# Kernel optimization log

Measured on AMD Instinct MI355X. Metric: run time of the kernel, lower is better.

The kernel has to match this reference:

```python
import jax, jax.numpy as jnp
import numpy as np
jax.config.update("jax_enable_x64", True)

B, S, E, H, L = 2, 1024, 768, 8, 8
FF, V = 2048, 32000
NT, REAL = 1, 512  # n_thoughts_taken, real_token_count


def _ln(x, g, b, eps=1e-5):
    m = jnp.mean(x, axis=-1, keepdims=True)
    v = jnp.var(x, axis=-1, keepdims=True)
    return (x - m) / jnp.sqrt(v + eps) * g + b


def setup_inputs() -> dict:
    key = jax.random.key(0)
    ks = jax.random.split(key, 12)
    f32 = jnp.float32
    rn = lambda k, shp, s=0.02: jax.random.normal(k, shp, f32) * s
    return {
        "x": jax.random.normal(ks[0], (B, S, E), f32),
        "tpe": rn(ks[1], (NT + 1, E)),
        "Wqkv": rn(ks[2], (L, 3 * E, E)),
        "bqkv": jnp.zeros((L, 3 * E), f32),
        "W1": rn(ks[3], (L, FF, E)),
        "b1": jnp.zeros((L, FF), f32),
        "W2": rn(ks[4], (L, E, FF)),
        "b2": jnp.zeros((L, E), f32),
        "g1": jnp.ones((L, E), f32),
        "be1": jnp.zeros((L, E), f32),
        "g2": jnp.ones((L, E), f32),
        "be2": jnp.zeros((L, E), f32),
        "gf": jnp.ones((E,), f32),
        "bf": jnp.zeros((E,), f32),
        "Wp1": rn(ks[5], (FF, E)),
        "bp1": jnp.zeros((FF,), f32),
        "Wp2": rn(ks[6], (V, FF)),
        "bp2": jnp.zeros((V,), f32),
        "Wv1": rn(ks[7], (FF, E)),
        "bv1": jnp.zeros((FF,), f32),
        "Wv2": rn(ks[8], (1, FF)),
        "bv2": jnp.zeros((1,), f32),
        "n_thoughts_taken": NT,
        "real_token_count": REAL,
    }


def reference(x, tpe, Wqkv, bqkv, W1, b1, W2, b2, g1, be1, g2, be2, gf, bf,
              Wp1, bp1, Wp2, bp2, Wv1, bv1, Wv2, bv2,
              n_thoughts_taken, real_token_count):
    Bs, Sq, Em = x.shape
    bs = int(n_thoughts_taken) + 1          # per-thought block size
    real = int(real_token_count)
    dh = Em // H

    # ---- DualPositionalEncoding (dropout=0) ----
    pos = np.arange(real)[:, None]
    div = np.exp(np.arange(0, Em, 2) * (-np.log(10000.0) / Em))
    pe = np.zeros((real, Em), np.float32)
    pe[:, 0::2] = np.sin(pos * div)
    pe[:, 1::2] = np.cos(pos * div)
    xb = x[:, :real * bs].reshape(Bs, real, bs, Em)
    xb = xb + jnp.asarray(pe)[None, :, None, :] + tpe[None, None, :bs, :]
    h = xb.reshape(Bs, real * bs, Em)
    pad = Sq - real * bs
    if pad > 0:
        h = jnp.pad(h, ((0, 0), (0, pad), (0, 0)))

    # ---- block-causal mask. NOTE: the original adds the BOOL mask to the
    # fp64 scores, so masked positions get +1.0 (not -inf). Faithful. ----
    i = np.arange(Sq)
    tok = i // bs
    p = i % bs
    M = ((tok[:, None] == tok[None, :]) & (p[None, :] >= p[:, None])) | \
        ((p[:, None] == 0) & (i[None, :] > i[:, None]) & (i[None, :] < real * bs))
    bias = jnp.asarray((M.T == 0).astype(np.float64))  # [S, S]
    scale = 1.0 / np.sqrt(dh)

    def layer(hc, params):
        Wq, bq, w1, b1_, w2, b2_, g1_, be1_, g2_, be2_ = params
        h64 = hc.astype(jnp.float64)
        qkv = h64 @ Wq.astype(jnp.float64).T + bq.astype(jnp.float64)
        q, k, v = jnp.split(qkv, 3, axis=-1)
        heads = lambda t: t.reshape(Bs, Sq, H, dh).transpose(0, 2, 1, 3)
        q, k, v = heads(q), heads(k), heads(v)
        scores = jnp.einsum('bhqd,bhkd->bhqk', q, k) * scale + bias
        w = jax.nn.softmax(scores, axis=-1)
        o = jnp.einsum('bhqk,bhkd->bhqd', w, v)
        o = o.transpose(0, 2, 1, 3).reshape(Bs, Sq, Em).astype(hc.dtype)
        # NOTE: original skips the attention out_proj entirely. Faithful.
        hc = _ln(hc + o, g1_, be1_)
        ff = jax.nn.gelu(hc @ w1.T + b1_, approximate=False) @ w2.T + b2_
        hc = _ln(hc + ff, g2_, be2_)
        return jnp.nan_to_num(hc), None

    h, _ = jax.lax.scan(layer, h, (Wqkv, bqkv, W1, b1, W2, b2, g1, be1, g2, be2))
    h = _ln(h, gf, bf)  # TransformerEncoder final norm

    act_idx = jnp.arange(real) * bs + n_thoughts_taken
    a = h[:, act_idx]  # [B, real, E]
    policy = jax.nn.gelu(a @ Wp1.T + bp1, approximate=False) @ Wp2.T + bp2
    value = jax.nn.gelu(a @ Wv1.T + bv1, approximate=False) @ Wv2.T + bv2
    return policy, value
```

## Files before the change

### kernel.cpp

```cpp
#include <hip/hip_runtime.h>
#include <math.h>

#define BB    2
#define SS    1024
#define EE    768
#define NH    8
#define DHD   96
#define NL    8
#define FFD   2048
#define VD    32000
#define REALC 512
#define MTOK  (BB*SS)
#define MACTN (BB*REALC)
#define QKVW  (3*EE)

#define QB 64
#define KB 64
#define KS_LD 104
#define VT_LD 72
#define P_LD  72

typedef __attribute__((ext_vector_type(8))) short bf16x8;
typedef __attribute__((ext_vector_type(4))) float f32x4;

static __device__ __forceinline__ float gelu_exact(float x) {
    return 0.5f * x * (1.0f + erff(x * 0.7071067811865476f));
}
static __device__ __forceinline__ unsigned short f2bf(float f) {
    unsigned int u = __builtin_bit_cast(unsigned int, f);
    unsigned int r = u + 0x7FFFu + ((u >> 16) & 1u);
    return (unsigned short)(r >> 16);
}
static __device__ __forceinline__ float bf2f(unsigned short u) {
    union { unsigned int i; float f; } v; v.i = ((unsigned int)u) << 16; return v.f;
}

#define GLDS16(gp, lp) __builtin_amdgcn_global_load_lds( \
    (const __attribute__((address_space(1))) void*)(gp), \
    (__attribute__((address_space(3))) void*)(lp), 16, 0, 0)

#define CN0 (NL*QKVW*EE)
#define CN1 (NL*FFD*EE)
#define CN2 (NL*EE*FFD)
#define CN3 (FFD*EE)
#define CN4 (FFD*EE)
#define CN5 (VD*FFD)
#define CB0 (CN0/4)
#define CB1 (CB0 + CN1/4)
#define CB2 (CB1 + CN2/4)
#define CB3 (CB2 + CN3/4)
#define CB4 (CB3 + CN4/4)
#define CB5 (CB4 + CN5/4)

__global__ __launch_bounds__(256) void convall_kernel(
    const float* __restrict__ s0, const float* __restrict__ s1,
    const float* __restrict__ s2, const float* __restrict__ s3,
    const float* __restrict__ s4, const float* __restrict__ s5,
    unsigned short* __restrict__ dst) {
    int i = blockIdx.x * 256 + threadIdx.x;
    const float* src;
    int loc;
    if      (i < CB0) { src = s0; loc = i; }
    else if (i < CB1) { src = s1; loc = i - CB0; }
    else if (i < CB2) { src = s2; loc = i - CB1; }
    else if (i < CB3) { src = s3; loc = i - CB2; }
    else if (i < CB4) { src = s4; loc = i - CB3; }
    else              { src = s5; loc = i - CB4; }
    float4 v = ((const float4*)src)[loc];
    ushort4 o;
    o.x = f2bf(v.x); o.y = f2bf(v.y); o.z = f2bf(v.z); o.w = f2bf(v.w);
    ((ushort4*)dst)[i] = o;
}

__global__ __launch_bounds__(256) void embed_kernel(const float* __restrict__ x,
                                                    const float* __restrict__ tpe,
                                                    float* __restrict__ h,
                                                    unsigned short* __restrict__ hb) {
    int idx = blockIdx.x * 256 + threadIdx.x;
    if (idx >= MTOK * EE) return;
    int e = idx % EE;
    int tok = idx / EE;
    int s = tok & (SS - 1);
    int r = s >> 1;
    int p = s & 1;
    int k2 = (e >> 1) * 2;
    double div = exp((double)k2 * (-9.210340371976184 / (double)EE));
    double ang = (double)r * div;
    float pe = (e & 1) ? (float)cos(ang) : (float)sin(ang);
    float v = x[idx] + pe + tpe[p * EE + e];
    h[idx] = v;
    hb[idx] = f2bf(v);
}

template<int MODE>
__global__ __launch_bounds__(256) void gemm64_kernel(
    const unsigned short* __restrict__ A, const unsigned short* __restrict__ W,
    const float* __restrict__ bias, float* __restrict__ Cf,
    unsigned short* __restrict__ Cb, unsigned short* __restrict__ CvT,
    int M, int N, int K, int ldc) {
    __shared__ unsigned short As[2][64 * 32];
    __shared__ unsigned short Bs[2][128 * 32];
    const int bm = blockIdx.y * 64;
    const int bn = blockIdx.x * 128;
    const int t = threadIdx.x;
    const int w = t >> 6;
    const int lane = t & 63;
    const int wm = (w >> 1) * 32;
    const int wn = (w & 1) * 64;
    f32x4 acc[2][4] = {};

    const int sr   = t >> 2;
    const int skey = (t >> 3) & 3;
    const int scol = ((t & 3) ^ skey) * 8;
    const unsigned short* gA = A + (size_t)(bm + sr) * K + scol;
    const unsigned short* gB = W + (size_t)(bn + sr) * K + scol;

    const int lc  = lane & 15;
    const int lr4 = lane >> 4;
    const int sl  = (lr4 ^ ((lc >> 1) & 3)) * 8;

    const int nsteps = K >> 5;
    GLDS16(gA,                  &As[0][w * 512]);
    GLDS16(gB,                  &Bs[0][w * 512]);
    GLDS16(gB + (size_t)64 * K, &Bs[0][2048 + w * 512]);
    __syncthreads();
    for (int kt = 0; kt < nsteps; ++kt) {
        const int cur = kt & 1;
        if (kt + 1 < nsteps) {
            const int k0 = (kt + 1) << 5;
            GLDS16(gA + k0,                  &As[cur ^ 1][w * 512]);
            GLDS16(gB + k0,                  &Bs[cur ^ 1][w * 512]);
            GLDS16(gB + (size_t)64 * K + k0, &Bs[cur ^ 1][2048 + w * 512]);
        }
        bf16x8 a[2], b[4];
#pragma unroll
        for (int mi = 0; mi < 2; ++mi)
            a[mi] = *(const bf16x8*)&As[cur][(wm + mi * 16 + lc) * 32 + sl];
#pragma unroll
        for (int ni = 0; ni < 4; ++ni)
            b[ni] = *(const bf16x8*)&Bs[cur][(wn + ni * 16 + lc) * 32 + sl];
#pragma unroll
        for (int mi = 0; mi < 2; ++mi)
#pragma unroll
            for (int ni = 0; ni < 4; ++ni)
                acc[mi][ni] = __builtin_amdgcn_mfma_f32_16x16x32_bf16(
                    a[mi], b[ni], acc[mi][ni], 0, 0, 0);
        __syncthreads();
    }

    const bool vpart = (MODE == 1) && (bn >= 2 * EE);
#pragma unroll
    for (int mi = 0; mi < 2; ++mi) {
#pragma unroll
        for (int ni = 0; ni < 4; ++ni) {
            const int c = bn + wn + ni * 16 + lc;
            const float bv = bias[c];
            const int rwb = bm + wm + mi * 16 + lr4 * 4;
            if (vpart) {
                ushort4 pk;
                pk.x = f2bf(acc[mi][ni][0] + bv);
                pk.y = f2bf(acc[mi][ni][1] + bv);
                pk.z = f2bf(acc[mi][ni][2] + bv);
                pk.w = f2bf(acc[mi][ni][3] + bv);
                *(ushort4*)&CvT[(size_t)(c - 2 * EE) * MTOK + rwb] = pk;
            } else {
#pragma unroll
                for (int r = 0; r < 4; ++r) {
                    float v = acc[mi][ni][r] + bv;
                    if (MODE == 3) {
                        v = gelu_exact(v);
                        Cb[(size_t)(rwb + r) * ldc + c] = f2bf(v);
                    } else if (MODE == 1) {
                        Cb[(size_t)(rwb + r) * ldc + c] = f2bf(v);
                    } else {
                        Cf[(size_t)(rwb + r) * ldc + c] = v;
                    }
                }
            }
        }
    }
}

__global__ __launch_bounds__(256, 2) void gemm_policy_kernel(
    const unsigned short* __restrict__ A, const unsigned short* __restrict__ W,
    const float* __restrict__ bias, float* __restrict__ C, int lda) {
    const int id = blockIdx.x;
    const int xcd = id & 7;
    const int rest = id >> 3;
    const int mt = rest & 7;
    const int ntile = (rest >> 3) * 8 + xcd;
    if (ntile >= VD / 256) return;
    const int bm = mt * 128;
    const int bn = ntile * 256;
    const int K = FFD;

    __shared__ unsigned short As[128 * 64];
    __shared__ unsigned short Bs[256 * 64];
    const int t = threadIdx.x;
    const int w = t >> 6;
    const int lane = t & 63;
    const int wm = (w >> 1) * 64;
    const int wn = (w & 1) * 128;
    f32x4 acc[4][8] = {};

    const int rr8  = (w << 3) + (lane >> 3);
    const int scol = (((lane & 7) ^ ((lane >> 3) & 7))) * 8;
    const unsigned short* gA = A + (size_t)(bm + rr8) * lda + scol;
    const unsigned short* gB = W + (size_t)(bn + rr8) * K + scol;

    const int lc  = lane & 15;
    const int lr4 = lane >> 4;
    const int key8 = lc & 7;

    for (int k0 = 0; k0 < K; k0 += 64) {
        __syncthreads();
#pragma unroll
        for (int i = 0; i < 4; ++i)
            GLDS16(gA + (size_t)(i * 32) * lda + k0, &As[((w << 3) + i * 32) * 64]);
#pragma unroll
        for (int i = 0; i < 8; ++i)
            GLDS16(gB + (size_t)(i * 32) * K + k0, &Bs[((w << 3) + i * 32) * 64]);
        __syncthreads();
#pragma unroll
        for (int ks = 0; ks < 2; ++ks) {
            const int sl = ((ks * 4 + lr4) ^ key8) * 8;
            bf16x8 a[4], b[8];
#pragma unroll
            for (int mi = 0; mi < 4; ++mi)
                a[mi] = *(const bf16x8*)&As[(wm + mi * 16 + lc) * 64 + sl];
#pragma unroll
            for (int ni = 0; ni < 8; ++ni)
                b[ni] = *(const bf16x8*)&Bs[(wn + ni * 16 + lc) * 64 + sl];
#pragma unroll
            for (int mi = 0; mi < 4; ++mi)
#pragma unroll
                for (int ni = 0; ni < 8; ++ni)
                    acc[mi][ni] = __builtin_amdgcn_mfma_f32_16x16x32_bf16(
                        a[mi], b[ni], acc[mi][ni], 0, 0, 0);
        }
    }
#pragma unroll
    for (int mi = 0; mi < 4; ++mi) {
#pragma unroll
        for (int ni = 0; ni < 8; ++ni) {
            const int c = bn + wn + ni * 16 + lc;
            const float bv = bias[c];
            const int rwb = bm + wm + mi * 16 + lr4 * 4;
#pragma unroll
            for (int r = 0; r < 4; ++r)
                C[(size_t)(rwb + r) * VD + c] = acc[mi][ni][r] + bv;
        }
    }
}

__global__ __launch_bounds__(256) void attn_mfma_kernel(
    const unsigned short* __restrict__ qkvb,
    const unsigned short* __restrict__ vT,
    float* __restrict__ o) {
    __shared__ unsigned short Ks[KB * KS_LD];
    __shared__ unsigned short VTs[DHD * VT_LD];
    __shared__ unsigned short Ps[QB * P_LD];

    const int bq = blockIdx.x * QB;
    const int hh = blockIdx.y & 7;
    const int b  = blockIdx.y >> 3;
    const int t = threadIdx.x;
    const int w = t >> 6;
    const int lane = t & 63;
    const int lr = lane >> 4;
    const int lc = lane & 15;
    const float scale = 0.10206207261596577f;

    bf16x8 qa[3];
    {
        const unsigned short* qrow = qkvb + (size_t)(b * SS + bq + w * 16 + lc) * QKVW + hh * DHD;
#pragma unroll
        for (int ks = 0; ks < 3; ++ks)
            qa[ks] = *(const bf16x8*)(qrow + ks * 32 + lr * 8);
    }

    f32x4 acc_o[6] = {};
    float m_st[4], l_st[4];
#pragma unroll
    for (int r = 0; r < 4; ++r) { m_st[r] = -1e30f; l_st[r] = 0.f; }
    const int q_row = lr << 2;

    for (int kt = 0; kt < SS / KB; ++kt) {
        __syncthreads();
#pragma unroll
        for (int it = 0; it < 3; ++it) {
            int flat = it * 256 + t;
            int kr = flat / 12;
            int d8 = (flat % 12) * 8;
            *(bf16x8*)&Ks[kr * KS_LD + d8] =
                *(const bf16x8*)&qkvb[(size_t)(b * SS + kt * KB + kr) * QKVW + EE + hh * DHD + d8];
            int d  = flat >> 3;
            int k8 = (flat & 7) * 8;
            *(bf16x8*)&VTs[d * VT_LD + k8] =
                *(const bf16x8*)&vT[(size_t)(hh * DHD + d) * MTOK + b * SS + kt * KB + k8];
        }
        __syncthreads();

        f32x4 sfr[4] = {};
#pragma unroll
        for (int nf = 0; nf < 4; ++nf) {
#pragma unroll
            for (int ks = 0; ks < 3; ++ks) {
                bf16x8 kb = *(const bf16x8*)&Ks[(nf * 16 + lc) * KS_LD + ks * 32 + lr * 8];
                sfr[nf] = __builtin_amdgcn_mfma_f32_16x16x32_bf16(qa[ks], kb, sfr[nf], 0, 0, 0);
            }
        }
        const int kbase = kt * KB;
#pragma unroll
        for (int nf = 0; nf < 4; ++nf) {
            const int k = kbase + nf * 16 + lc;
#pragma unroll
            for (int r = 0; r < 4; ++r) {
                const int q = bq + w * 16 + q_row + r;
                bool allowed = (((k >> 1) == (q >> 1)) && ((q & 1) >= (k & 1))) ||
                               (((k & 1) == 0) && (q > k));
                sfr[nf][r] = sfr[nf][r] * scale + (allowed ? 0.f : 1.f);
            }
        }
        float corr[4];
#pragma unroll
        for (int r = 0; r < 4; ++r) {
            float v = fmaxf(fmaxf(sfr[0][r], sfr[1][r]), fmaxf(sfr[2][r], sfr[3][r]));
            v = fmaxf(v, __shfl_xor(v, 1)); v = fmaxf(v, __shfl_xor(v, 2));
            v = fmaxf(v, __shfl_xor(v, 4)); v = fmaxf(v, __shfl_xor(v, 8));
            float mn = fmaxf(m_st[r], v);
            corr[r] = __expf(m_st[r] - mn);
            m_st[r] = mn;
        }
        float rsum[4] = {0.f, 0.f, 0.f, 0.f};
#pragma unroll
        for (int nf = 0; nf < 4; ++nf) {
#pragma unroll
            for (int r = 0; r < 4; ++r) {
                float p = __expf(sfr[nf][r] - m_st[r]);
                rsum[r] += p;
                Ps[(w * 16 + q_row + r) * P_LD + nf * 16 + lc] = f2bf(p);
            }
        }
#pragma unroll
        for (int r = 0; r < 4; ++r) {
            float v = rsum[r];
            v += __shfl_xor(v, 1); v += __shfl_xor(v, 2);
            v += __shfl_xor(v, 4); v += __shfl_xor(v, 8);
            l_st[r] = l_st[r] * corr[r] + v;
        }
#pragma unroll
        for (int nf = 0; nf < 6; ++nf)
#pragma unroll
            for (int r = 0; r < 4; ++r)
                acc_o[nf][r] *= corr[r];
#pragma unroll
        for (int ks2 = 0; ks2 < 2; ++ks2) {
            bf16x8 pa = *(const bf16x8*)&Ps[(w * 16 + lc) * P_LD + ks2 * 32 + lr * 8];
#pragma unroll
            for (int nf = 0; nf < 6; ++nf) {
                bf16x8 vb = *(const bf16x8*)&VTs[(nf * 16 + lc) * VT_LD + ks2 * 32 + lr * 8];
                acc_o[nf] = __builtin_amdgcn_mfma_f32_16x16x32_bf16(pa, vb, acc_o[nf], 0, 0, 0);
            }
        }
    }
#pragma unroll
    for (int nf = 0; nf < 6; ++nf) {
#pragma unroll
        for (int r = 0; r < 4; ++r) {
            const int q = bq + w * 16 + q_row + r;
            o[(size_t)(b * SS + q) * EE + hh * DHD + nf * 16 + lc] = acc_o[nf][r] / l_st[r];
        }
    }
}

template<bool GATHER>
__global__ __launch_bounds__(256) void ln_kernel(const float* __restrict__ a,
                                                 const float* __restrict__ res,
                                                 const float* __restrict__ g,
                                                 const float* __restrict__ beta,
                                                 float* __restrict__ outf,
                                                 unsigned short* __restrict__ outb) {
    __shared__ float rs[256], rs2[256];
    const int row = blockIdx.x;
    const int t = threadIdx.x;
    int src = row;
    if (GATHER) src = (row >> 9) * SS + ((row & 511) << 1) + 1;
    const float* pa = a + (size_t)src * EE;
    const float* pr = res ? res + (size_t)src * EE : nullptr;
    float x[3];
    float s = 0.f, s2 = 0.f;
#pragma unroll
    for (int i = 0; i < 3; ++i) {
        int e = t + i * 256;
        float v = pa[e] + (pr ? pr[e] : 0.f);
        x[i] = v; s += v; s2 += v * v;
    }
    rs[t] = s; rs2[t] = s2; __syncthreads();
    for (int k = 128; k > 0; k >>= 1) {
        if (t < k) { rs[t] += rs[t + k]; rs2[t] += rs2[t + k]; }
        __syncthreads();
    }
    const float mean = rs[0] * (1.0f / EE);
    const float var  = rs2[0] * (1.0f / EE) - mean * mean;
    const float rstd = 1.0f / sqrtf(var + 1e-5f);
#pragma unroll
    for (int i = 0; i < 3; ++i) {
        int e = t + i * 256;
        float v = (x[i] - mean) * rstd * g[e] + beta[e];
        if (isnan(v)) v = 0.f;
        if (outf) outf[(size_t)row * EE + e] = v;
        if (outb) outb[(size_t)row * EE + e] = f2bf(v);
    }
}

__global__ __launch_bounds__(256) void value2_kernel(const unsigned short* __restrict__ v1,
                                                     const float* __restrict__ Wv2,
                                                     const float* __restrict__ bv2,
                                                     float* __restrict__ out, int ld) {
    __shared__ float red[256];
    const int row = blockIdx.x;
    const int t = threadIdx.x;
    const unsigned short* pr = v1 + (size_t)row * ld;
    float s = 0.f;
    for (int i = t; i < FFD; i += 256) s = fmaf(bf2f(pr[i]), Wv2[i], s);
    red[t] = s; __syncthreads();
    for (int k = 128; k > 0; k >>= 1) {
        if (t < k) red[t] += red[t + k];
        __syncthreads();
    }
    if (t == 0) out[row] = red[0] + bv2[0];
}

extern "C" void kernel_launch(void* const* d_in, const int* in_sizes, int n_in,
                              void* d_out, int out_size, void* d_ws, size_t ws_size,
                              hipStream_t stream) {
    const float* x    = (const float*)d_in[0];
    const float* tpe  = (const float*)d_in[1];
    const float* Wqkv = (const float*)d_in[2];
    const float* bqkv = (const float*)d_in[3];
    const float* W1   = (const float*)d_in[4];
    const float* b1   = (const float*)d_in[5];
    const float* W2   = (const float*)d_in[6];
    const float* b2   = (const float*)d_in[7];
    const float* g1   = (const float*)d_in[8];
    const float* be1  = (const float*)d_in[9];
    const float* g2   = (const float*)d_in[10];
    const float* be2  = (const float*)d_in[11];
    const float* gf   = (const float*)d_in[12];
    const float* bf   = (const float*)d_in[13];
    const float* Wp1  = (const float*)d_in[14];
    const float* bp1  = (const float*)d_in[15];
    const float* Wp2  = (const float*)d_in[16];
    const float* bp2  = (const float*)d_in[17];
    const float* Wv1  = (const float*)d_in[18];
    const float* bv1  = (const float*)d_in[19];
    const float* Wv2  = (const float*)d_in[20];
    const float* bv2  = (const float*)d_in[21];

    float* ws  = (float*)d_ws;
    float* h   = ws;
    float* o   = h  + (size_t)MTOK * EE;
    float* hc  = o  + (size_t)MTOK * EE;
    float* ff2 = hc + (size_t)MTOK * EE;
    float* bias_cat = ff2 + (size_t)MTOK * EE;
    unsigned short* bws = (unsigned short*)(bias_cat + 4096);
    unsigned short* h_bf    = bws;
    unsigned short* hc_bf   = h_bf    + (size_t)MTOK * EE;
    unsigned short* ff1_bf  = hc_bf   + (size_t)MTOK * EE;
    unsigned short* act_bf  = ff1_bf  + (size_t)MTOK * FFD;
    unsigned short* p1v1_bf = act_bf  + (size_t)MACTN * EE;
    unsigned short* qkv_bf  = p1v1_bf + (size_t)MACTN * 2 * FFD;
    unsigned short* vT      = qkv_bf  + (size_t)MTOK * QKVW;
    unsigned short* wq_all  = vT      + (size_t)EE * MTOK;
    unsigned short* w1_all  = wq_all  + (size_t)CN0;
    unsigned short* w2_all  = w1_all  + (size_t)CN1;
    unsigned short* wp1_bf  = w2_all  + (size_t)CN2;
    unsigned short* wv1_bf  = wp1_bf  + (size_t)CN3;
    unsigned short* wp2_bf  = wv1_bf  + (size_t)CN4;
    (void)wv1_bf;

    float* pol = (float*)d_out;
    float* val = (float*)d_out + (size_t)MACTN * VD;

    const int C256 = 256;
#define NBLK(n) (((n) + 255) / 256)

    embed_kernel<<<NBLK(MTOK * EE), C256, 0, stream>>>(x, tpe, h, h_bf);

    convall_kernel<<<CB5 / 256, C256, 0, stream>>>(Wqkv, W1, W2, Wp1, Wv1, Wp2, wq_all);

    hipMemcpyAsync(bias_cat,        bp1, FFD * sizeof(float), hipMemcpyDeviceToDevice, stream);
    hipMemcpyAsync(bias_cat + FFD,  bv1, FFD * sizeof(float), hipMemcpyDeviceToDevice, stream);

    for (int l = 0; l < NL; ++l) {
        gemm64_kernel<1><<<dim3(QKVW / 128, MTOK / 64), C256, 0, stream>>>(
            h_bf, wq_all + (size_t)l * QKVW * EE, bqkv + (size_t)l * QKVW,
            nullptr, qkv_bf, vT, MTOK, QKVW, EE, QKVW);
        attn_mfma_kernel<<<dim3(SS / QB, BB * NH), C256, 0, stream>>>(qkv_bf, vT, o);
        ln_kernel<false><<<MTOK, C256, 0, stream>>>(h, o, g1 + l * EE, be1 + l * EE, hc, hc_bf);
        gemm64_kernel<3><<<dim3(FFD / 128, MTOK / 64), C256, 0, stream>>>(
            hc_bf, w1_all + (size_t)l * FFD * EE, b1 + (size_t)l * FFD,
            nullptr, ff1_bf, nullptr, MTOK, FFD, EE, FFD);
        gemm64_kernel<0><<<dim3(EE / 128, MTOK / 64), C256, 0, stream>>>(
            ff1_bf, w2_all + (size_t)l * EE * FFD, b2 + (size_t)l * EE,
            ff2, nullptr, nullptr, MTOK, EE, FFD, EE);
        ln_kernel<false><<<MTOK, C256, 0, stream>>>(hc, ff2, g2 + l * EE, be2 + l * EE, h, h_bf);
    }

    ln_kernel<true><<<MACTN, C256, 0, stream>>>(h, nullptr, gf, bf, nullptr, act_bf);

    gemm64_kernel<3><<<dim3(2 * FFD / 128, MACTN / 64), C256, 0, stream>>>(
        act_bf, wp1_bf, bias_cat, nullptr, p1v1_bf, nullptr, MACTN, 2 * FFD, EE, 2 * FFD);

    gemm_policy_kernel<<<1024, C256, 0, stream>>>(p1v1_bf, wp2_bf, bp2, pol, 2 * FFD);

    value2_kernel<<<MACTN, C256, 0, stream>>>(p1v1_bf + FFD, Wv2, bv2, val, 2 * FFD);
#undef NBLK
}
```

Baseline: 1.324 ms.

## Split-K the FF2 GEMM and fold partial sums plus bias into layernorm

```diff
diff --git a/kernel.cpp b/kernel.cpp
--- a/kernel.cpp
+++ b/kernel.cpp
@@ -97,7 +97,7 @@
     const unsigned short* __restrict__ A, const unsigned short* __restrict__ W,
     const float* __restrict__ bias, float* __restrict__ Cf,
     unsigned short* __restrict__ Cb, unsigned short* __restrict__ CvT,
-    int M, int N, int K, int ldc) {
+    int M, int N, int K, int lda, int ldb, int ldc) {
     __shared__ unsigned short As[2][64 * 32];
     __shared__ unsigned short Bs[2][128 * 32];
     const int bm = blockIdx.y * 64;
@@ -109,28 +109,30 @@
     const int wn = (w & 1) * 64;
     f32x4 acc[2][4] = {};
 
+    const size_t koff = (MODE == 4) ? (size_t)blockIdx.z * K : 0;
+
     const int sr   = t >> 2;
     const int skey = (t >> 3) & 3;
     const int scol = ((t & 3) ^ skey) * 8;
-    const unsigned short* gA = A + (size_t)(bm + sr) * K + scol;
-    const unsigned short* gB = W + (size_t)(bn + sr) * K + scol;
+    const unsigned short* gA = A + (size_t)(bm + sr) * lda + koff + scol;
+    const unsigned short* gB = W + (size_t)(bn + sr) * ldb + koff + scol;
 
     const int lc  = lane & 15;
     const int lr4 = lane >> 4;
     const int sl  = (lr4 ^ ((lc >> 1) & 3)) * 8;
 
     const int nsteps = K >> 5;
-    GLDS16(gA,                  &As[0][w * 512]);
-    GLDS16(gB,                  &Bs[0][w * 512]);
-    GLDS16(gB + (size_t)64 * K, &Bs[0][2048 + w * 512]);
+    GLDS16(gA,                    &As[0][w * 512]);
+    GLDS16(gB,                    &Bs[0][w * 512]);
+    GLDS16(gB + (size_t)64 * ldb, &Bs[0][2048 + w * 512]);
     __syncthreads();
     for (int kt = 0; kt < nsteps; ++kt) {
         const int cur = kt & 1;
         if (kt + 1 < nsteps) {
             const int k0 = (kt + 1) << 5;
-            GLDS16(gA + k0,                  &As[cur ^ 1][w * 512]);
-            GLDS16(gB + k0,                  &Bs[cur ^ 1][w * 512]);
-            GLDS16(gB + (size_t)64 * K + k0, &Bs[cur ^ 1][2048 + w * 512]);
+            GLDS16(gA + k0,                    &As[cur ^ 1][w * 512]);
+            GLDS16(gB + k0,                    &Bs[cur ^ 1][w * 512]);
+            GLDS16(gB + (size_t)64 * ldb + k0, &Bs[cur ^ 1][2048 + w * 512]);
         }
         bf16x8 a[2], b[4];
 #pragma unroll
@@ -148,13 +150,14 @@
         __syncthreads();
     }
 
+    float* Cfp = (MODE == 4) ? Cf + (size_t)blockIdx.z * M * ldc : Cf;
     const bool vpart = (MODE == 1) && (bn >= 2 * EE);
 #pragma unroll
     for (int mi = 0; mi < 2; ++mi) {
 #pragma unroll
         for (int ni = 0; ni < 4; ++ni) {
             const int c = bn + wn + ni * 16 + lc;
-            const float bv = bias[c];
+            const float bv = (MODE == 4) ? 0.f : bias[c];
             const int rwb = bm + wm + mi * 16 + lr4 * 4;
             if (vpart) {
                 ushort4 pk;
@@ -173,7 +176,7 @@
                     } else if (MODE == 1) {
                         Cb[(size_t)(rwb + r) * ldc + c] = f2bf(v);
                     } else {
-                        Cf[(size_t)(rwb + r) * ldc + c] = v;
+                        Cfp[(size_t)(rwb + r) * ldc + c] = v;
                     }
                 }
             }
@@ -284,6 +287,7 @@
 #pragma unroll
     for (int r = 0; r < 4; ++r) { m_st[r] = -1e30f; l_st[r] = 0.f; }
     const int q_row = lr << 2;
+    const int qbase = bq + w * 16 + q_row;
 
     for (int kt = 0; kt < SS / KB; ++kt) {
         __syncthreads();
@@ -314,11 +318,11 @@
 #pragma unroll
         for (int nf = 0; nf < 4; ++nf) {
             const int k = kbase + nf * 16 + lc;
+            const bool kodd = (k & 1);
 #pragma unroll
             for (int r = 0; r < 4; ++r) {
-                const int q = bq + w * 16 + q_row + r;
-                bool allowed = (((k >> 1) == (q >> 1)) && ((q & 1) >= (k & 1))) ||
-                               (((k & 1) == 0) && (q > k));
+                const int q = qbase + r;
+                bool allowed = kodd ? (q == k) : (q >= k);
                 sfr[nf][r] = sfr[nf][r] * scale + (allowed ? 0.f : 1.f);
             }
         }
@@ -376,9 +380,11 @@
 
 template<bool GATHER>
 __global__ __launch_bounds__(256) void ln_kernel(const float* __restrict__ a,
-                                                 const float* __restrict__ res,
+                                                 const float* __restrict__ parts,
+                                                 size_t pstride, int nparts,
                                                  const float* __restrict__ g,
                                                  const float* __restrict__ beta,
+                                                 const float* __restrict__ bias2,
                                                  float* __restrict__ outf,
                                                  unsigned short* __restrict__ outb) {
     __shared__ float rs[256], rs2[256];
@@ -387,13 +393,14 @@
     int src = row;
     if (GATHER) src = (row >> 9) * SS + ((row & 511) << 1) + 1;
     const float* pa = a + (size_t)src * EE;
-    const float* pr = res ? res + (size_t)src * EE : nullptr;
     float x[3];
     float s = 0.f, s2 = 0.f;
 #pragma unroll
     for (int i = 0; i < 3; ++i) {
         int e = t + i * 256;
-        float v = pa[e] + (pr ? pr[e] : 0.f);
+        float v = pa[e] + (bias2 ? bias2[e] : 0.f);
+        for (int p = 0; p < nparts; ++p)
+            v += parts[p * pstride + (size_t)src * EE + e];
         x[i] = v; s += v; s2 += v * v;
     }
     rs[t] = s; rs2[t] = s2; __syncthreads();
@@ -459,11 +466,11 @@
     const float* bv2  = (const float*)d_in[21];
 
     float* ws  = (float*)d_ws;
-    float* h   = ws;
-    float* o   = h  + (size_t)MTOK * EE;
-    float* hc  = o  + (size_t)MTOK * EE;
-    float* ff2 = hc + (size_t)MTOK * EE;
-    float* bias_cat = ff2 + (size_t)MTOK * EE;
+    float* h    = ws;
+    float* o    = h   + (size_t)MTOK * EE;
+    float* hc   = o   + (size_t)MTOK * EE;
+    float* ff2p = hc  + (size_t)MTOK * EE;
+    float* bias_cat = ff2p + (size_t)4 * MTOK * EE;
     unsigned short* bws = (unsigned short*)(bias_cat + 4096);
     unsigned short* h_bf    = bws;
     unsigned short* hc_bf   = h_bf    + (size_t)MTOK * EE;
@@ -496,22 +503,27 @@
     for (int l = 0; l < NL; ++l) {
         gemm64_kernel<1><<<dim3(QKVW / 128, MTOK / 64), C256, 0, stream>>>(
             h_bf, wq_all + (size_t)l * QKVW * EE, bqkv + (size_t)l * QKVW,
-            nullptr, qkv_bf, vT, MTOK, QKVW, EE, QKVW);
+            nullptr, qkv_bf, vT, MTOK, QKVW, EE, EE, EE, QKVW);
         attn_mfma_kernel<<<dim3(SS / QB, BB * NH), C256, 0, stream>>>(qkv_bf, vT, o);
-        ln_kernel<false><<<MTOK, C256, 0, stream>>>(h, o, g1 + l * EE, be1 + l * EE, hc, hc_bf);
+        ln_kernel<false><<<MTOK, C256, 0, stream>>>(
+            h, o, 0, 1, g1 + l * EE, be1 + l * EE, nullptr, hc, hc_bf);
         gemm64_kernel<3><<<dim3(FFD / 128, MTOK / 64), C256, 0, stream>>>(
             hc_bf, w1_all + (size_t)l * FFD * EE, b1 + (size_t)l * FFD,
-            nullptr, ff1_bf, nullptr, MTOK, FFD, EE, FFD);
-        gemm64_kernel<0><<<dim3(EE / 128, MTOK / 64), C256, 0, stream>>>(
-            ff1_bf, w2_all + (size_t)l * EE * FFD, b2 + (size_t)l * EE,
-            ff2, nullptr, nullptr, MTOK, EE, FFD, EE);
-        ln_kernel<false><<<MTOK, C256, 0, stream>>>(hc, ff2, g2 + l * EE, be2 + l * EE, h, h_bf);
-    }
-
-    ln_kernel<true><<<MACTN, C256, 0, stream>>>(h, nullptr, gf, bf, nullptr, act_bf);
+            nullptr, ff1_bf, nullptr, MTOK, FFD, EE, EE, EE, FFD);
+        gemm64_kernel<4><<<dim3(EE / 128, MTOK / 64, 4), C256, 0, stream>>>(
+            ff1_bf, w2_all + (size_t)l * EE * FFD, nullptr,
+            ff2p, nullptr, nullptr, MTOK, EE, FFD / 4, FFD, FFD, EE);
+        ln_kernel<false><<<MTOK, C256, 0, stream>>>(
+            hc, ff2p, (size_t)MTOK * EE, 4, g2 + l * EE, be2 + l * EE,
+            b2 + (size_t)l * EE, h, h_bf);
+    }
+
+    ln_kernel<true><<<MACTN, C256, 0, stream>>>(
+        h, nullptr, 0, 0, gf, bf, nullptr, nullptr, act_bf);
 
     gemm64_kernel<3><<<dim3(2 * FFD / 128, MACTN / 64), C256, 0, stream>>>(
-        act_bf, wp1_bf, bias_cat, nullptr, p1v1_bf, nullptr, MACTN, 2 * FFD, EE, 2 * FFD);
+        act_bf, wp1_bf, bias_cat, nullptr, p1v1_bf, nullptr,
+        MACTN, 2 * FFD, EE, EE, EE, 2 * FFD);
 
     gemm_policy_kernel<<<1024, C256, 0, stream>>>(p1v1_bf, wp2_bf, bp2, pol, 2 * FFD);
 
```

After: 1.432 ms. +8.2%, slower.

## Double-buffer K/V tiles in attention kernel with register prefetch

Applied to the files above, without the earlier changes.

```diff
diff --git a/kernel.cpp b/kernel.cpp
--- a/kernel.cpp
+++ b/kernel.cpp
@@ -257,8 +257,8 @@
     const unsigned short* __restrict__ qkvb,
     const unsigned short* __restrict__ vT,
     float* __restrict__ o) {
-    __shared__ unsigned short Ks[KB * KS_LD];
-    __shared__ unsigned short VTs[DHD * VT_LD];
+    __shared__ unsigned short Ks[2][KB * KS_LD];
+    __shared__ unsigned short VTs[2][DHD * VT_LD];
     __shared__ unsigned short Ps[QB * P_LD];
 
     const int bq = blockIdx.x * QB;
@@ -271,6 +271,22 @@
     const int lc = lane & 15;
     const float scale = 0.10206207261596577f;
 
+    const unsigned short* gK[3];
+    const unsigned short* gV[3];
+    int kwr[3], vwr[3];
+#pragma unroll
+    for (int it = 0; it < 3; ++it) {
+        int flat = it * 256 + t;
+        int kr = flat / 12;
+        int d8 = (flat % 12) * 8;
+        int d  = flat >> 3;
+        int k8 = (flat & 7) * 8;
+        gK[it] = qkvb + (size_t)(b * SS + kr) * QKVW + EE + hh * DHD + d8;
+        gV[it] = vT + (size_t)(hh * DHD + d) * MTOK + b * SS + k8;
+        kwr[it] = kr * KS_LD + d8;
+        vwr[it] = d * VT_LD + k8;
+    }
+
     bf16x8 qa[3];
     {
         const unsigned short* qrow = qkvb + (size_t)(b * SS + bq + w * 16 + lc) * QKVW + hh * DHD;
@@ -284,29 +300,38 @@
 #pragma unroll
     for (int r = 0; r < 4; ++r) { m_st[r] = -1e30f; l_st[r] = 0.f; }
     const int q_row = lr << 2;
-
-    for (int kt = 0; kt < SS / KB; ++kt) {
-        __syncthreads();
-#pragma unroll
-        for (int it = 0; it < 3; ++it) {
-            int flat = it * 256 + t;
-            int kr = flat / 12;
-            int d8 = (flat % 12) * 8;
-            *(bf16x8*)&Ks[kr * KS_LD + d8] =
-                *(const bf16x8*)&qkvb[(size_t)(b * SS + kt * KB + kr) * QKVW + EE + hh * DHD + d8];
-            int d  = flat >> 3;
-            int k8 = (flat & 7) * 8;
-            *(bf16x8*)&VTs[d * VT_LD + k8] =
-                *(const bf16x8*)&vT[(size_t)(hh * DHD + d) * MTOK + b * SS + kt * KB + k8];
-        }
-        __syncthreads();
+    const int qbase = bq + w * 16 + q_row;
+
+    bf16x8 kst[3], vst[3];
+#pragma unroll
+    for (int it = 0; it < 3; ++it) {
+        kst[it] = *(const bf16x8*)gK[it];
+        vst[it] = *(const bf16x8*)gV[it];
+    }
+#pragma unroll
+    for (int it = 0; it < 3; ++it) {
+        *(bf16x8*)&Ks[0][kwr[it]] = kst[it];
+        *(bf16x8*)&VTs[0][vwr[it]] = vst[it];
+    }
+    __syncthreads();
+
+    const int NTILE = SS / KB;
+    for (int kt = 0; kt < NTILE; ++kt) {
+        const int cur = kt & 1;
+        if (kt + 1 < NTILE) {
+#pragma unroll
+            for (int it = 0; it < 3; ++it) {
+                kst[it] = *(const bf16x8*)(gK[it] + (size_t)(kt + 1) * KB * QKVW);
+                vst[it] = *(const bf16x8*)(gV[it] + (kt + 1) * KB);
+            }
+        }
 
         f32x4 sfr[4] = {};
 #pragma unroll
         for (int nf = 0; nf < 4; ++nf) {
 #pragma unroll
             for (int ks = 0; ks < 3; ++ks) {
-                bf16x8 kb = *(const bf16x8*)&Ks[(nf * 16 + lc) * KS_LD + ks * 32 + lr * 8];
+                bf16x8 kb = *(const bf16x8*)&Ks[cur][(nf * 16 + lc) * KS_LD + ks * 32 + lr * 8];
                 sfr[nf] = __builtin_amdgcn_mfma_f32_16x16x32_bf16(qa[ks], kb, sfr[nf], 0, 0, 0);
             }
         }
@@ -314,11 +339,11 @@
 #pragma unroll
         for (int nf = 0; nf < 4; ++nf) {
             const int k = kbase + nf * 16 + lc;
+            const bool kodd = (k & 1);
 #pragma unroll
             for (int r = 0; r < 4; ++r) {
-                const int q = bq + w * 16 + q_row + r;
-                bool allowed = (((k >> 1) == (q >> 1)) && ((q & 1) >= (k & 1))) ||
-                               (((k & 1) == 0) && (q > k));
+                const int q = qbase + r;
+                bool allowed = kodd ? (q == k) : (q >= k);
                 sfr[nf][r] = sfr[nf][r] * scale + (allowed ? 0.f : 1.f);
             }
         }
@@ -359,10 +384,19 @@
             bf16x8 pa = *(const bf16x8*)&Ps[(w * 16 + lc) * P_LD + ks2 * 32 + lr * 8];
 #pragma unroll
             for (int nf = 0; nf < 6; ++nf) {
-                bf16x8 vb = *(const bf16x8*)&VTs[(nf * 16 + lc) * VT_LD + ks2 * 32 + lr * 8];
+                bf16x8 vb = *(const bf16x8*)&VTs[cur][(nf * 16 + lc) * VT_LD + ks2 * 32 + lr * 8];
                 acc_o[nf] = __builtin_amdgcn_mfma_f32_16x16x32_bf16(pa, vb, acc_o[nf], 0, 0, 0);
             }
         }
+
+        if (kt + 1 < NTILE) {
+#pragma unroll
+            for (int it = 0; it < 3; ++it) {
+                *(bf16x8*)&Ks[cur ^ 1][kwr[it]] = kst[it];
+                *(bf16x8*)&VTs[cur ^ 1][vwr[it]] = vst[it];
+            }
+        }
+        __syncthreads();
     }
 #pragma unroll
     for (int nf = 0; nf < 6; ++nf) {
```

After: 1.286 ms. 1.03x faster.
